# Kernel optimization log

Hardware: AMD Instinct MI355X
Metric: run time of the kernel (lower is better)

The kernel has to match this reference:

```python
import jax, jax.numpy as jnp
import numpy as np

DIM = 64  # head dim, init arg
SCALE = DIM ** -0.5

def setup_inputs() -> dict:
    key = jax.random.key(0)
    kq, kk, kv = jax.random.split(key, 3)
    shape = (4, 2048, 8, 64)  # (b, n, h, d)
    q = jax.random.normal(kq, shape, dtype=jnp.float32)
    k = jax.random.normal(kk, shape, dtype=jnp.float32)
    v = jax.random.normal(kv, shape, dtype=jnp.float32)
    return {"q": q, "k": k, "v": v}

def reference(q, k, v):
    # score: [b, h, n_q, n_k] -- matches torch bmm over (b*h) batched [n, d] x [d, n]
    score = jnp.einsum('bqhd,bkhd->bhqk', q, k) * SCALE
    attn = jax.nn.softmax(score, axis=-1)
    # context back to [b, n, h, d] (torch permutes h,b,n,d -> b,n,h,d)
    context = jnp.einsum('bhqk,bkhd->bqhd', attn, v)
    return context
```

## Files before the change

### kernel.cpp

```cpp
#include <hip/hip_runtime.h>

#define B 4
#define N 2048
#define H 8
#define D 64
#define HD 512
#define QT 128
#define KT 64
#define NTILES (N / KT)
#define PLS 72

typedef _Float16 half8 __attribute__((ext_vector_type(8)));
typedef _Float16 half4 __attribute__((ext_vector_type(4)));
typedef float float4_ __attribute__((ext_vector_type(4)));

__global__ void prep_kernel(const float* __restrict__ K, const float* __restrict__ V,
                            _Float16* __restrict__ Kf, _Float16* __restrict__ Vtr) {
    __shared__ _Float16 tile[64][PLS];
    const int t = threadIdx.x;
    if (blockIdx.x < 2048) {
        const size_t i = (size_t)blockIdx.x * 256 + t;
        const float4_* p = (const float4_*)(K + i * 8);
        float4_ a = p[0], b = p[1];
        half8 hh;
        #pragma unroll
        for (int j = 0; j < 4; ++j) { hh[j] = (_Float16)a[j]; hh[4 + j] = (_Float16)b[j]; }
        *(half8*)(Kf + i * 8) = hh;
    } else {
        const int bid = blockIdx.x - 2048;
        const int nt = bid & 31, h = (bid >> 5) & 7, b = bid >> 8;
        {
            const int i = t >> 2, c0 = (t & 3) * 16;
            const float* vp = V + (size_t)b * N * HD + (size_t)(nt * 64 + i) * HD + h * D + c0;
            #pragma unroll
            for (int j = 0; j < 4; ++j) {
                float4_ a = *(const float4_*)(vp + j * 4);
                #pragma unroll
                for (int c = 0; c < 4; ++c) tile[i][c0 + j * 4 + c] = (_Float16)a[c];
            }
        }
        __syncthreads();
        {
            const int d = t >> 2, n0 = (t & 3) * 16;
            half8 lo, hi;
            #pragma unroll
            for (int j = 0; j < 8; ++j) { lo[j] = tile[n0 + j][d]; hi[j] = tile[n0 + 8 + j][d]; }
            _Float16* op = Vtr + ((size_t)(b * H + h) * D + d) * N + nt * 64 + n0;
            *(half8*)op = lo;
            *(half8*)(op + 8) = hi;
        }
    }
}

__device__ __forceinline__ void stage_k(const _Float16* __restrict__ Kbh, int keybase,
                                        _Float16* kb, int wave, int lane) {
    const int rsub = lane >> 3, slot = lane & 7;
    #pragma unroll
    for (int i = 0; i < 2; ++i) {
        const int row = wave * 16 + i * 8 + rsub;
        const int c = slot ^ (row & 7);
        __builtin_amdgcn_global_load_lds(
            (const __attribute__((address_space(1))) void*)(Kbh + (size_t)(keybase + row) * HD + c * 8),
            (__attribute__((address_space(3))) void*)(kb + (wave * 16 + i * 8) * 64), 16, 0, 0);
    }
}
__device__ __forceinline__ void stage_v(const _Float16* __restrict__ Vbh, int keybase,
                                        _Float16* vb, int wave, int lane) {
    const int rsub = lane >> 3, slot = lane & 7;
    #pragma unroll
    for (int i = 0; i < 2; ++i) {
        const int row = wave * 16 + i * 8 + rsub;
        const int c = slot ^ (row & 7);
        __builtin_amdgcn_global_load_lds(
            (const __attribute__((address_space(1))) void*)(Vbh + (size_t)row * N + keybase + c * 8),
            (__attribute__((address_space(3))) void*)(vb + (wave * 16 + i * 8) * 64), 16, 0, 0);
    }
}

__device__ __forceinline__ void do_st(const _Float16* Kt, const half8 qf[2][2],
                                      float lsum[2], _Float16* PwW, int m, int quad) {
    #pragma unroll
    for (int blk = 0; blk < 4; ++blk) {
        const int key = blk * 16 + m;
        half8 kf0 = *(const half8*)(Kt + key * 64 + ((quad ^ (m & 7)) * 8));
        half8 kf1 = *(const half8*)(Kt + key * 64 + (((4 + quad) ^ (m & 7)) * 8));
        #pragma unroll
        for (int u = 0; u < 2; ++u) {
            float4_ acc = {};
            acc = __builtin_amdgcn_mfma_f32_16x16x32_f16(kf0, qf[u][0], acc, 0, 0, 0);
            acc = __builtin_amdgcn_mfma_f32_16x16x32_f16(kf1, qf[u][1], acc, 0, 0, 0);
            half4 pk;
            #pragma unroll
            for (int r = 0; r < 4; ++r) {
                float p = __builtin_amdgcn_exp2f(acc[r]);
                lsum[u] += p;
                pk[r] = (_Float16)p;
            }
            const int kpos = (blk * 16 + quad * 4) ^ ((m & 7) << 3);
            *(half4*)(PwW + (u * 16 + m) * 64 + kpos) = pk;
        }
    }
}

__device__ __forceinline__ void load_af(half8 af[2][2], const _Float16* PwW, int m, int quad) {
    #pragma unroll
    for (int u = 0; u < 2; ++u)
        #pragma unroll
        for (int ks = 0; ks < 2; ++ks)
            af[u][ks] = *(const half8*)(PwW + (u * 16 + m) * 64
                                        + ((ks * 32 + quad * 8) ^ ((m & 7) << 3)));
}

__device__ __forceinline__ void do_pv(const _Float16* Vtile, const half8 af[2][2],
                                      float4_ o[2][4], int m, int quad) {
    #pragma unroll
    for (int ks = 0; ks < 2; ++ks)
        #pragma unroll
        for (int db = 0; db < 4; ++db) {
            half8 bf = *(const half8*)(Vtile + (db * 16 + m) * 64
                                       + ((((ks << 2) + quad) ^ (m & 7)) * 8));
            #pragma unroll
            for (int u = 0; u < 2; ++u)
                o[u][db] = __builtin_amdgcn_mfma_f32_16x16x32_f16(af[u][ks], bf, o[u][db], 0, 0, 0);
        }
}

__global__ __launch_bounds__(256, 2)
void fattn5_kernel(const float* __restrict__ Q, const _Float16* __restrict__ Kf,
                   const _Float16* __restrict__ Vt, float* __restrict__ Out)
{
    __shared__ __align__(16) _Float16 Kb[2][KT * 64];
    __shared__ __align__(16) _Float16 Vb[2][D * 64];
    __shared__ __align__(16) _Float16 Pw[4][32 * 64];

    const int tid  = threadIdx.x;
    const int wave = tid >> 6;
    const int lane = tid & 63;
    const int m    = lane & 15;
    const int quad = lane >> 4;

    const int h = blockIdx.y;
    const int b = blockIdx.z;
    const int q_base = blockIdx.x * QT + wave * 32;

    const size_t bh_q = (size_t)b * N * HD + (size_t)h * D;
    const _Float16* Kbh = Kf + bh_q;
    const _Float16* Vbh = Vt + (size_t)(b * H + h) * D * N;
    _Float16* PwW = Pw[wave];

    const float SC = 0.125f * 1.4426950408889634f;
    half8 qf[2][2];
    #pragma unroll
    for (int u = 0; u < 2; ++u) {
        const float* qp = Q + bh_q + (size_t)(q_base + u * 16 + m) * HD + quad * 8;
        float4_ a0 = *(const float4_*)qp,        a1 = *(const float4_*)(qp + 4);
        float4_ b0 = *(const float4_*)(qp + 32), b1 = *(const float4_*)(qp + 36);
        #pragma unroll
        for (int jj = 0; jj < 4; ++jj) {
            qf[u][0][jj] = (_Float16)(a0[jj] * SC); qf[u][0][4 + jj] = (_Float16)(a1[jj] * SC);
            qf[u][1][jj] = (_Float16)(b0[jj] * SC); qf[u][1][4 + jj] = (_Float16)(b1[jj] * SC);
        }
    }

    float4_ o[2][4] = {};
    float lsum[2] = {0.f, 0.f};

    stage_k(Kbh, 0, Kb[0], wave, lane);
    __syncthreads();
    stage_k(Kbh, KT, Kb[1], wave, lane);
    stage_v(Vbh, 0, Vb[0], wave, lane);
    do_st(Kb[0], qf, lsum, PwW, m, quad);

    for (int t = 1; t < NTILES; ++t) {
        __syncthreads();
        if (t + 1 < NTILES)
            stage_k(Kbh, (t + 1) * KT, Kb[(t + 1) & 1], wave, lane);
        stage_v(Vbh, t * KT, Vb[t & 1], wave, lane);

        half8 af[2][2];
        load_af(af, PwW, m, quad);
        do_st(Kb[t & 1], qf, lsum, PwW, m, quad);
        do_pv(Vb[(t - 1) & 1], af, o, m, quad);
    }

    __syncthreads();
    {
        half8 af[2][2];
        load_af(af, PwW, m, quad);
        do_pv(Vb[(NTILES - 1) & 1], af, o, m, quad);
    }

    float inv[2];
    #pragma unroll
    for (int u = 0; u < 2; ++u) {
        float v = lsum[u];
        v += __shfl_xor(v, 16, 64);
        v += __shfl_xor(v, 32, 64);
        inv[u] = 1.0f / v;
    }
    #pragma unroll
    for (int u = 0; u < 2; ++u) {
        #pragma unroll
        for (int r = 0; r < 4; ++r) {
            const int src = (lane & 48) | (quad * 4 + r);
            const float linv = __shfl(inv[u], src, 64);
            const int row = q_base + u * 16 + quad * 4 + r;
            #pragma unroll
            for (int db = 0; db < 4; ++db)
                Out[bh_q + (size_t)row * HD + db * 16 + m] = o[u][db][r] * linv;
        }
    }
}

__global__ __launch_bounds__(256, 2)
void fattn_fb_kernel(const float* __restrict__ Q, const float* __restrict__ K,
                     const float* __restrict__ V, float* __restrict__ Out)
{
    __shared__ __align__(16) _Float16 Ks[KT][PLS];
    __shared__ __align__(16) _Float16 Vts[D][PLS];
    __shared__ __align__(16) _Float16 Pwf[4][16][PLS];
    const int tid = threadIdx.x, wave = tid >> 6, lane = tid & 63;
    const int m = lane & 15, quad = lane >> 4;
    const int q_base = blockIdx.x * 64;
    const size_t bh_off = ((size_t)blockIdx.z * N * H + (size_t)blockIdx.y) * D;
    const float SCALE = 0.125f;
    const int qrow = q_base + wave * 16 + m;
    const float* qp = Q + bh_off + (size_t)qrow * HD + quad * 8;
    half8 qf0, qf1;
    #pragma unroll
    for (int j = 0; j < 8; ++j) qf0[j] = (_Float16)(qp[j] * SCALE);
    #pragma unroll
    for (int j = 0; j < 8; ++j) qf1[j] = (_Float16)(qp[32 + j] * SCALE);
    float4_ o[4] = {};
    float mi[4], li[4];
    #pragma unroll
    for (int r = 0; r < 4; ++r) { mi[r] = -1e30f; li[r] = 0.0f; }
    for (int kt = 0; kt < N; kt += KT) {
        __syncthreads();
        {
            const int key = tid >> 2, c0 = (tid & 3) * 16;
            const float* kp = K + bh_off + (size_t)(kt + key) * HD + c0;
            half8 lo, hi;
            #pragma unroll
            for (int j = 0; j < 8; ++j) lo[j] = (_Float16)kp[j];
            #pragma unroll
            for (int j = 0; j < 8; ++j) hi[j] = (_Float16)kp[8 + j];
            *(half8*)&Ks[key][c0] = lo;
            *(half8*)&Ks[key][c0 + 8] = hi;
        }
        {
            const int c0 = (tid & 15) * 4, k0 = (tid >> 4) * 4;
            const float* vp = V + bh_off + (size_t)(kt + k0) * HD + c0;
            #pragma unroll
            for (int c = 0; c < 4; ++c)
                #pragma unroll
                for (int i = 0; i < 4; ++i)
                    Vts[c0 + c][k0 + i] = (_Float16)vp[i * HD + c];
        }
        __syncthreads();
        float4_ s[4];
        #pragma unroll
        for (int blk = 0; blk < 4; ++blk) {
            const int key = blk * 16 + m;
            half8 kf0 = *(const half8*)&Ks[key][quad * 8];
            half8 kf1 = *(const half8*)&Ks[key][32 + quad * 8];
            float4_ acc = {};
            acc = __builtin_amdgcn_mfma_f32_16x16x32_f16(qf0, kf0, acc, 0, 0, 0);
            acc = __builtin_amdgcn_mfma_f32_16x16x32_f16(qf1, kf1, acc, 0, 0, 0);
            s[blk] = acc;
        }
        float alpha[4];
        #pragma unroll
        for (int r = 0; r < 4; ++r) {
            float v0 = fmaxf(fmaxf(s[0][r], s[1][r]), fmaxf(s[2][r], s[3][r]));
            #pragma unroll
            for (int mask = 1; mask < 16; mask <<= 1) v0 = fmaxf(v0, __shfl_xor(v0, mask, 64));
            float mn = fmaxf(mi[r], v0);
            alpha[r] = __expf(mi[r] - mn);
            mi[r] = mn;
        }
        #pragma unroll
        for (int blk = 0; blk < 4; ++blk)
            #pragma unroll
            for (int r = 0; r < 4; ++r) s[blk][r] = __expf(s[blk][r] - mi[r]);
        #pragma unroll
        for (int r = 0; r < 4; ++r) {
            float tt = s[0][r] + s[1][r] + s[2][r] + s[3][r];
            #pragma unroll
            for (int mask = 1; mask < 16; mask <<= 1) tt += __shfl_xor(tt, mask, 64);
            li[r] = li[r] * alpha[r] + tt;
        }
        #pragma unroll
        for (int d = 0; d < 4; ++d)
            #pragma unroll
            for (int r = 0; r < 4; ++r) o[d][r] *= alpha[r];
        #pragma unroll
        for (int blk = 0; blk < 4; ++blk)
            #pragma unroll
            for (int r = 0; r < 4; ++r)
                Pwf[wave][quad * 4 + r][blk * 16 + m] = (_Float16)s[blk][r];
        #pragma unroll
        for (int ks = 0; ks < 2; ++ks) {
            half8 af = *(const half8*)&Pwf[wave][m][ks * 32 + quad * 8];
            #pragma unroll
            for (int d = 0; d < 4; ++d) {
                half8 bf = *(const half8*)&Vts[d * 16 + m][ks * 32 + quad * 8];
                o[d] = __builtin_amdgcn_mfma_f32_16x16x32_f16(af, bf, o[d], 0, 0, 0);
            }
        }
    }
    #pragma unroll
    for (int d = 0; d < 4; ++d)
        #pragma unroll
        for (int r = 0; r < 4; ++r) {
            const int row = q_base + wave * 16 + quad * 4 + r;
            Out[bh_off + (size_t)row * HD + d * 16 + m] = o[d][r] / li[r];
        }
}

extern "C" void kernel_launch(void* const* d_in, const int* in_sizes, int n_in,
                              void* d_out, int out_size, void* d_ws, size_t ws_size,
                              hipStream_t stream) {
    const float* q = (const float*)d_in[0];
    const float* k = (const float*)d_in[1];
    const float* v = (const float*)d_in[2];
    float* out = (float*)d_out;

    const size_t nelem = (size_t)B * N * H * D;
    const size_t need = 2 * nelem * sizeof(_Float16);

    if (ws_size >= need) {
        _Float16* Kf = (_Float16*)d_ws;
        _Float16* Vtr = Kf + nelem;
        prep_kernel<<<dim3(2048 + 1024), 256, 0, stream>>>(k, v, Kf, Vtr);
        fattn5_kernel<<<dim3(N / QT, H, B), 256, 0, stream>>>(q, Kf, Vtr, out);
    } else {
        fattn_fb_kernel<<<dim3(N / 64, H, B), 256, 0, stream>>>(q, k, v, out);
    }
}
```

Measured before the change: 139.9 us.

## Switch attention to 32x32x16 MFMA computing S^T so P stays in registers

Replaces the 16x16x32 MFMA formulation with 32x32x16 MFMAs that compute the transposed score tile. The output layout then matches the A-operand layout for the PV product, so exp'd probabilities feed the next MFMA straight from registers. The per-wave LDS staging buffer for P and its reloads go away, and the V transpose in the prep kernel is permuted to match the new key ordering. It also adds s_setprio around the MFMA blocks, at the cost of larger accumulator register usage per wave.

```diff
diff --git a/kernel.cpp b/kernel.cpp
--- a/kernel.cpp
+++ b/kernel.cpp
@@ -11,8 +11,8 @@
 #define PLS 72
 
 typedef _Float16 half8 __attribute__((ext_vector_type(8)));
-typedef _Float16 half4 __attribute__((ext_vector_type(4)));
 typedef float float4_ __attribute__((ext_vector_type(4)));
+typedef float float16_ __attribute__((ext_vector_type(16)));
 
 __global__ void prep_kernel(const float* __restrict__ K, const float* __restrict__ V,
                             _Float16* __restrict__ Kf, _Float16* __restrict__ Vtr) {
@@ -42,12 +42,17 @@
         __syncthreads();
         {
             const int d = t >> 2, n0 = (t & 3) * 16;
-            half8 lo, hi;
-            #pragma unroll
-            for (int j = 0; j < 8; ++j) { lo[j] = tile[n0 + j][d]; hi[j] = tile[n0 + 8 + j][d]; }
+            half8 w0, w1;
+            #pragma unroll
+            for (int j = 0; j < 4; ++j) {
+                w0[j]     = tile[n0 + j][d];
+                w0[4 + j] = tile[n0 + 8 + j][d];
+                w1[j]     = tile[n0 + 4 + j][d];
+                w1[4 + j] = tile[n0 + 12 + j][d];
+            }
             _Float16* op = Vtr + ((size_t)(b * H + h) * D + d) * N + nt * 64 + n0;
-            *(half8*)op = lo;
-            *(half8*)(op + 8) = hi;
+            *(half8*)op = w0;
+            *(half8*)(op + 8) = w1;
         }
     }
 }
@@ -77,67 +82,64 @@
     }
 }
 
-__device__ __forceinline__ void do_st(const _Float16* Kt, const half8 qf[2][2],
-                                      float lsum[2], _Float16* PwW, int m, int quad) {
-    #pragma unroll
-    for (int blk = 0; blk < 4; ++blk) {
-        const int key = blk * 16 + m;
-        half8 kf0 = *(const half8*)(Kt + key * 64 + ((quad ^ (m & 7)) * 8));
-        half8 kf1 = *(const half8*)(Kt + key * 64 + (((4 + quad) ^ (m & 7)) * 8));
-        #pragma unroll
-        for (int u = 0; u < 2; ++u) {
-            float4_ acc = {};
-            acc = __builtin_amdgcn_mfma_f32_16x16x32_f16(kf0, qf[u][0], acc, 0, 0, 0);
-            acc = __builtin_amdgcn_mfma_f32_16x16x32_f16(kf1, qf[u][1], acc, 0, 0, 0);
-            half4 pk;
-            #pragma unroll
-            for (int r = 0; r < 4; ++r) {
-                float p = __builtin_amdgcn_exp2f(acc[r]);
-                lsum[u] += p;
-                pk[r] = (_Float16)p;
-            }
-            const int kpos = (blk * 16 + quad * 4) ^ ((m & 7) << 3);
-            *(half4*)(PwW + (u * 16 + m) * 64 + kpos) = pk;
-        }
-    }
-}
-
-__device__ __forceinline__ void load_af(half8 af[2][2], const _Float16* PwW, int m, int quad) {
-    #pragma unroll
-    for (int u = 0; u < 2; ++u)
-        #pragma unroll
-        for (int ks = 0; ks < 2; ++ks)
-            af[u][ks] = *(const half8*)(PwW + (u * 16 + m) * 64
-                                        + ((ks * 32 + quad * 8) ^ ((m & 7) << 3)));
-}
-
-__device__ __forceinline__ void do_pv(const _Float16* Vtile, const half8 af[2][2],
-                                      float4_ o[2][4], int m, int quad) {
-    #pragma unroll
-    for (int ks = 0; ks < 2; ++ks)
-        #pragma unroll
-        for (int db = 0; db < 4; ++db) {
-            half8 bf = *(const half8*)(Vtile + (db * 16 + m) * 64
-                                       + ((((ks << 2) + quad) ^ (m & 7)) * 8));
-            #pragma unroll
-            for (int u = 0; u < 2; ++u)
-                o[u][db] = __builtin_amdgcn_mfma_f32_16x16x32_f16(af[u][ks], bf, o[u][db], 0, 0, 0);
-        }
+static __device__ __forceinline__ void do_s(const _Float16* __restrict__ Kt,
+                                            const half8 qf[4], float& lsum,
+                                            half8 pf[4], int ln, int hi) {
+    float16_ s0 = {}, s1 = {};
+    __builtin_amdgcn_s_setprio(1);
+    #pragma unroll
+    for (int ks = 0; ks < 4; ++ks) {
+        const int csw = ((2 * ks + hi) ^ (ln & 7)) * 8;
+        half8 a0 = *(const half8*)(Kt + ln * 64 + csw);
+        half8 a1 = *(const half8*)(Kt + (32 + ln) * 64 + csw);
+        s0 = __builtin_amdgcn_mfma_f32_32x32x16_f16(a0, qf[ks], s0, 0, 0, 0);
+        s1 = __builtin_amdgcn_mfma_f32_32x32x16_f16(a1, qf[ks], s1, 0, 0, 0);
+    }
+    __builtin_amdgcn_s_setprio(0);
+    #pragma unroll
+    for (int kb = 0; kb < 2; ++kb) {
+        const float16_ s = kb ? s1 : s0;
+        half8 f0, f1;
+        #pragma unroll
+        for (int j = 0; j < 8; ++j) {
+            float pa = __builtin_amdgcn_exp2f(s[j]);
+            float pb = __builtin_amdgcn_exp2f(s[8 + j]);
+            lsum += pa + pb;
+            f0[j] = (_Float16)pa;
+            f1[j] = (_Float16)pb;
+        }
+        pf[2 * kb]     = f0;
+        pf[2 * kb + 1] = f1;
+    }
+}
+
+static __device__ __forceinline__ void do_pv(const _Float16* __restrict__ Vtile,
+                                             const half8 pf[4], float16_& o0, float16_& o1,
+                                             int ln, int hi) {
+    __builtin_amdgcn_s_setprio(1);
+    #pragma unroll
+    for (int ks = 0; ks < 4; ++ks) {
+        const int csw = ((2 * ks + hi) ^ (ln & 7)) * 8;
+        half8 b0 = *(const half8*)(Vtile + ln * 64 + csw);
+        half8 b1 = *(const half8*)(Vtile + (32 + ln) * 64 + csw);
+        o0 = __builtin_amdgcn_mfma_f32_32x32x16_f16(pf[ks], b0, o0, 0, 0, 0);
+        o1 = __builtin_amdgcn_mfma_f32_32x32x16_f16(pf[ks], b1, o1, 0, 0, 0);
+    }
+    __builtin_amdgcn_s_setprio(0);
 }
 
 __global__ __launch_bounds__(256, 2)
-void fattn5_kernel(const float* __restrict__ Q, const _Float16* __restrict__ Kf,
+void fattn7_kernel(const float* __restrict__ Q, const _Float16* __restrict__ Kf,
                    const _Float16* __restrict__ Vt, float* __restrict__ Out)
 {
     __shared__ __align__(16) _Float16 Kb[2][KT * 64];
     __shared__ __align__(16) _Float16 Vb[2][D * 64];
-    __shared__ __align__(16) _Float16 Pw[4][32 * 64];
 
     const int tid  = threadIdx.x;
     const int wave = tid >> 6;
     const int lane = tid & 63;
-    const int m    = lane & 15;
-    const int quad = lane >> 4;
+    const int ln   = lane & 31;
+    const int hi   = lane >> 5;
 
     const int h = blockIdx.y;
     const int b = blockIdx.z;
@@ -146,30 +148,31 @@
     const size_t bh_q = (size_t)b * N * HD + (size_t)h * D;
     const _Float16* Kbh = Kf + bh_q;
     const _Float16* Vbh = Vt + (size_t)(b * H + h) * D * N;
-    _Float16* PwW = Pw[wave];
 
     const float SC = 0.125f * 1.4426950408889634f;
-    half8 qf[2][2];
-    #pragma unroll
-    for (int u = 0; u < 2; ++u) {
-        const float* qp = Q + bh_q + (size_t)(q_base + u * 16 + m) * HD + quad * 8;
-        float4_ a0 = *(const float4_*)qp,        a1 = *(const float4_*)(qp + 4);
-        float4_ b0 = *(const float4_*)(qp + 32), b1 = *(const float4_*)(qp + 36);
-        #pragma unroll
-        for (int jj = 0; jj < 4; ++jj) {
-            qf[u][0][jj] = (_Float16)(a0[jj] * SC); qf[u][0][4 + jj] = (_Float16)(a1[jj] * SC);
-            qf[u][1][jj] = (_Float16)(b0[jj] * SC); qf[u][1][4 + jj] = (_Float16)(b1[jj] * SC);
-        }
-    }
-
-    float4_ o[2][4] = {};
-    float lsum[2] = {0.f, 0.f};
+    half8 qf[4];
+    {
+        const float* qp = Q + bh_q + (size_t)(q_base + ln) * HD + hi * 8;
+        #pragma unroll
+        for (int ks = 0; ks < 4; ++ks) {
+            float4_ a0 = *(const float4_*)(qp + ks * 16);
+            float4_ a1 = *(const float4_*)(qp + ks * 16 + 4);
+            half8 f;
+            #pragma unroll
+            for (int j = 0; j < 4; ++j) { f[j] = (_Float16)(a0[j] * SC); f[4 + j] = (_Float16)(a1[j] * SC); }
+            qf[ks] = f;
+        }
+    }
+
+    float16_ o0 = {}, o1 = {};
+    float lsum = 0.f;
+    half8 pf[4];
 
     stage_k(Kbh, 0, Kb[0], wave, lane);
     __syncthreads();
     stage_k(Kbh, KT, Kb[1], wave, lane);
     stage_v(Vbh, 0, Vb[0], wave, lane);
-    do_st(Kb[0], qf, lsum, PwW, m, quad);
+    do_s(Kb[0], qf, lsum, pf, ln, hi);
 
     for (int t = 1; t < NTILES; ++t) {
         __syncthreads();
@@ -177,38 +180,22 @@
             stage_k(Kbh, (t + 1) * KT, Kb[(t + 1) & 1], wave, lane);
         stage_v(Vbh, t * KT, Vb[t & 1], wave, lane);
 
-        half8 af[2][2];
-        load_af(af, PwW, m, quad);
-        do_st(Kb[t & 1], qf, lsum, PwW, m, quad);
-        do_pv(Vb[(t - 1) & 1], af, o, m, quad);
+        do_pv(Vb[(t - 1) & 1], pf, o0, o1, ln, hi);
+        do_s(Kb[t & 1], qf, lsum, pf, ln, hi);
     }
 
     __syncthreads();
-    {
-        half8 af[2][2];
-        load_af(af, PwW, m, quad);
-        do_pv(Vb[(NTILES - 1) & 1], af, o, m, quad);
-    }
-
-    float inv[2];
-    #pragma unroll
-    for (int u = 0; u < 2; ++u) {
-        float v = lsum[u];
-        v += __shfl_xor(v, 16, 64);
-        v += __shfl_xor(v, 32, 64);
-        inv[u] = 1.0f / v;
-    }
-    #pragma unroll
-    for (int u = 0; u < 2; ++u) {
-        #pragma unroll
-        for (int r = 0; r < 4; ++r) {
-            const int src = (lane & 48) | (quad * 4 + r);
-            const float linv = __shfl(inv[u], src, 64);
-            const int row = q_base + u * 16 + quad * 4 + r;
-            #pragma unroll
-            for (int db = 0; db < 4; ++db)
-                Out[bh_q + (size_t)row * HD + db * 16 + m] = o[u][db][r] * linv;
-        }
+    do_pv(Vb[(NTILES - 1) & 1], pf, o0, o1, ln, hi);
+
+    lsum += __shfl_xor(lsum, 32, 64);
+    const float inv = 1.0f / lsum;
+    #pragma unroll
+    for (int r = 0; r < 16; ++r) {
+        const int rl = (r & 3) + 8 * (r >> 2) + 4 * hi;
+        const float linv = __shfl(inv, rl, 64);
+        const size_t ro = bh_q + (size_t)(q_base + rl) * HD;
+        Out[ro + ln]      = o0[r] * linv;
+        Out[ro + 32 + ln] = o1[r] * linv;
     }
 }
 
@@ -333,7 +320,7 @@
         _Float16* Kf = (_Float16*)d_ws;
         _Float16* Vtr = Kf + nelem;
         prep_kernel<<<dim3(2048 + 1024), 256, 0, stream>>>(k, v, Kf, Vtr);
-        fattn5_kernel<<<dim3(N / QT, H, B), 256, 0, stream>>>(q, Kf, Vtr, out);
+        fattn7_kernel<<<dim3(N / QT, H, B), 256, 0, stream>>>(q, Kf, Vtr, out);
     } else {
         fattn_fb_kernel<<<dim3(N / 64, H, B), 256, 0, stream>>>(q, k, v, out);
     }
```

After: 136.4 us. 2.5% less time.
